# Performance work log

Hardware: AMD Instinct MI355X
Metric: run time of the kernel (lower is better)

## Reference

```python
import jax, jax.numpy as jnp
import numpy as np

N, R, D = 2048, 4, 256
TEMPERATURE = 1.0
CLAMP_MIN = 1e-8


def setup_inputs() -> dict:
    key = jax.random.key(0)
    a = jax.random.normal(key, (N, R, D), dtype=jnp.float32)
    return {"a": a}


def reference(a):
    n, r, d = a.shape
    # Full pairwise Gram tensor over (input i, context j) x (input k, context l)
    sim = jnp.einsum('ijd,kld->ikjl', a, a) / TEMPERATURE          # [N,N,r,r]
    # detached row-max over l for stability (matches sim.detach().max(-1, keepdim=True))
    sim_max = jax.lax.stop_gradient(jnp.max(sim, axis=-1, keepdims=True))
    dp = jnp.exp(sim - sim_max)                                    # [N,N,r,r]

    # Positive pairs: i == k, j != l
    diag = jnp.einsum('iijl->ijl', dp)                             # [N,r,r]
    offdiag_jl = ~jnp.eye(r, dtype=bool)                           # [r,r]
    sim_pos = jnp.sum(diag * offdiag_jl, axis=(1, 2)) / (r * (r - 1))  # [N]

    # Negative pairs: i != k, all (j,l); square then clamp, then per-i mean
    sq = jnp.maximum(jnp.square(dp), CLAMP_MIN)                    # [N,N,r,r]
    diag_sq = jnp.sum(jnp.maximum(jnp.square(diag), CLAMP_MIN), axis=(1, 2))  # [N]
    sim_neg = (jnp.sum(sq, axis=(1, 2, 3)) - diag_sq) / ((n - 1) * r * r)     # [N]

    lora_loss = -2.0 * sim_pos + sim_neg                           # [N]
    return jnp.mean(lora_loss)                                     # 'mean' reduction -> scalar
```

## Files before the change

### kernel.cpp

```cpp
#include <hip/hip_runtime.h>


#define PD   8192
#define KB   256
#define BM   128
#define BK   32
#define NIT  (KB / BK)

typedef __bf16 bf16x8 __attribute__((ext_vector_type(8)));
typedef float f32x4 __attribute__((ext_vector_type(4)));

__device__ __forceinline__ void gload16(const void* g, void* l) {
    __builtin_amdgcn_global_load_lds(
        (const __attribute__((address_space(1))) unsigned int*)g,
        (__attribute__((address_space(3))) unsigned int*)l, 16, 0, 0);
}

__device__ __forceinline__ int swz(int row) { return ((row >> 1) & 3) << 4; }

__device__ __forceinline__ float quadmax(float x) {
    int v = __builtin_amdgcn_mov_dpp(__builtin_bit_cast(int, x), 0xB1, 0xF, 0xF, true);
    float m = fmaxf(x, __builtin_bit_cast(float, v));
    v = __builtin_amdgcn_mov_dpp(__builtin_bit_cast(int, m), 0x4E, 0xF, 0xF, true);
    return fmaxf(m, __builtin_bit_cast(float, v));
}

__global__ __launch_bounds__(256)
void cvt_bf16(const float* __restrict__ A, __bf16* __restrict__ W,
              float* __restrict__ out) {
    const int idx = blockIdx.x * 256 + threadIdx.x;
    if (idx == 0) *out = 0.f;
    const float4 v0 = reinterpret_cast<const float4*>(A)[idx * 2];
    const float4 v1 = reinterpret_cast<const float4*>(A)[idx * 2 + 1];
    bf16x8 h;
    h[0] = (__bf16)v0.x; h[1] = (__bf16)v0.y; h[2] = (__bf16)v0.z; h[3] = (__bf16)v0.w;
    h[4] = (__bf16)v1.x; h[5] = (__bf16)v1.y; h[6] = (__bf16)v1.z; h[7] = (__bf16)v1.w;
    *reinterpret_cast<bf16x8*>(W + (size_t)idx * 8) = h;
}

__global__ __launch_bounds__(256)
void evd_mfma(const __bf16* __restrict__ W, float* __restrict__ out)
{
    __shared__ __bf16 lds[2][2][BM * BK];
    __shared__ float wsum[4];

    const int x = blockIdx.x, y = blockIdx.y;
    int bi, bk;
    if (x < 64 - y) { bi = y;      bk = y + x; }
    else            { bi = 63 - y; bk = x - 1; }

    const int tid = threadIdx.x;
    const int lane = tid & 63, wid = tid >> 6;
    const int wr = wid >> 1, wc = wid & 1;
    const int row0 = bi * BM, col0 = bk * BM;

    const int r0 = tid >> 2;
    const int r1 = 64 + r0;
    const int x0 = (tid & 3) * 16;
    const int ga0 = r0 * (KB * 2) + (x0 ^ swz(r0));
    const int ga1 = r1 * (KB * 2) + (x0 ^ swz(r1));
    const char* gAb = (const char*)(W + (size_t)row0 * KB);
    const char* gBb = (const char*)(W + (size_t)col0 * KB);
    const int ldsOff0 = wid * 1024;
    const int ldsOff1 = 4096 + wid * 1024;

    const int fr = lane & 15, kq = lane >> 4;
    int aOff[4], bOff[4];
#pragma unroll
    for (int m = 0; m < 4; ++m) {
        const int ra = wr * 64 + m * 16 + fr;
        const int rb = wc * 64 + m * 16 + fr;
        aOff[m] = ra * 64 + ((kq * 16) ^ swz(ra));
        bOff[m] = rb * 64 + ((kq * 16) ^ swz(rb));
    }

    f32x4 acc[4][4];
#pragma unroll
    for (int m = 0; m < 4; ++m)
#pragma unroll
        for (int n = 0; n < 4; ++n)
#pragma unroll
            for (int q = 0; q < 4; ++q) acc[m][n][q] = 0.f;

    auto stage = [&](int t, int b) {
        const int kbyte = t * (BK * 2);
        char* dA = (char*)&lds[b][0][0];
        char* dB = (char*)&lds[b][1][0];
        gload16(gAb + ga0 + kbyte, dA + ldsOff0);
        gload16(gAb + ga1 + kbyte, dA + ldsOff1);
        gload16(gBb + ga0 + kbyte, dB + ldsOff0);
        gload16(gBb + ga1 + kbyte, dB + ldsOff1);
    };

    stage(0, 0);
    stage(1, 1);

#pragma unroll
    for (int t = 0; t < NIT; ++t) {
        if (t == NIT - 1) asm volatile("s_waitcnt vmcnt(0)" ::: "memory");
        else              asm volatile("s_waitcnt vmcnt(4)" ::: "memory");
        __builtin_amdgcn_s_barrier();

        const char* baseA = (const char*)&lds[t & 1][0][0];
        const char* baseB = (const char*)&lds[t & 1][1][0];
        bf16x8 af[4], bfr[4];
#pragma unroll
        for (int m = 0; m < 4; ++m) {
            af[m]  = *(const bf16x8*)(baseA + aOff[m]);
            bfr[m] = *(const bf16x8*)(baseB + bOff[m]);
        }
        if (t + 2 < NIT) {
            asm volatile("s_waitcnt lgkmcnt(0)" ::: "memory");
            __builtin_amdgcn_s_barrier();
            stage(t + 2, t & 1);
        }
#pragma unroll
        for (int m = 0; m < 4; ++m)
#pragma unroll
            for (int n = 0; n < 4; ++n)
                acc[m][n] = __builtin_amdgcn_mfma_f32_16x16x32_bf16(af[m], bfr[n], acc[m][n], 0, 0, 0);
    }

    const float C_NEG = 1.0f / (2048.0f * 2047.0f * 16.0f);
    const float C_POS = 2.0f / (2048.0f * 12.0f);
    const float SCL = 2.0f * 1.4426950408889634f;
    const bool diag = (bi == bk);
    const bool ik = ((lane >> 4) == ((lane & 15) >> 2));
    float nsum = 0.f, psum = 0.f;

#pragma unroll
    for (int m = 0; m < 4; ++m) {
#pragma unroll
        for (int n = 0; n < 4; ++n) {
            float yv[4];
#pragma unroll
            for (int q = 0; q < 4; ++q) yv[q] = SCL * acc[m][n][q];
            const bool dfrag = diag && (wr == wc) && (m == n);
#pragma unroll
            for (int r = 0; r < 4; ++r) {
                const float d2 = yv[r] - quadmax(yv[r]);
                if (dfrag) {
                    const float dp = __builtin_amdgcn_exp2f(0.5f * d2);
                    if (ik) {
                        if (r != (lane & 3)) psum += dp;
                    } else {
                        nsum += fmaxf(dp * dp, 1e-8f);
                    }
                } else {
                    nsum += fmaxf(__builtin_amdgcn_exp2f(d2), 1e-8f);
                }
            }
            if (!diag) {
                const float ymax = fmaxf(fmaxf(fmaxf(yv[0], yv[1]), yv[2]), yv[3]);
#pragma unroll
                for (int r = 0; r < 4; ++r)
                    nsum += fmaxf(__builtin_amdgcn_exp2f(yv[r] - ymax), 1e-8f);
            }
        }
    }

    float contrib = C_NEG * nsum - C_POS * psum;

#pragma unroll
    for (int off = 32; off; off >>= 1) contrib += __shfl_down(contrib, off);
    if ((tid & 63) == 0) wsum[tid >> 6] = contrib;
    __syncthreads();
    if (tid == 0) atomicAdd(out, wsum[0] + wsum[1] + wsum[2] + wsum[3]);
}

extern "C" void kernel_launch(void* const* d_in, const int* in_sizes, int n_in,
                              void* d_out, int out_size, void* d_ws, size_t ws_size,
                              hipStream_t stream) {
    const float* A = (const float*)d_in[0];
    float* out = (float*)d_out;
    __bf16* W = (__bf16*)d_ws;
    cvt_bf16<<<(PD * KB / 8) / 256, 256, 0, stream>>>(A, W, out);
    dim3 grid(65, 32);
    evd_mfma<<<grid, 256, 0, stream>>>(W, out);
}
```

Baseline: 98.96 us.

## Use 8-wave blocks with 64x32 warp tiles, XCD-aware block remap, MFMA priority

Each 128x128 tile block now runs 8 waves instead of 4, and each wave computes a 64x32 sub-tile, which halves per-wave accumulators and increases latency hiding. The grid is flattened to 1D and remapped so consecutive blocks spread across the XCDs in chunks, aiming for better L2 locality. s_setprio is raised around the MFMA loop. Staging is simplified to one load per operand per thread. The cost is more waves contending for LDS and barriers, and a more complex epilogue diagonal test.

```diff
diff --git a/kernel.cpp b/kernel.cpp
--- a/kernel.cpp
+++ b/kernel.cpp
@@ -38,58 +38,49 @@
     *reinterpret_cast<bf16x8*>(W + (size_t)idx * 8) = h;
 }
 
-__global__ __launch_bounds__(256)
+__global__ __launch_bounds__(512, 4)
 void evd_mfma(const __bf16* __restrict__ W, float* __restrict__ out)
 {
     __shared__ __bf16 lds[2][2][BM * BK];
-    __shared__ float wsum[4];
+    __shared__ float wsum[8];
 
-    const int x = blockIdx.x, y = blockIdx.y;
+    const int nid = blockIdx.x;
+    const int id  = (nid & 7) * 260 + (nid >> 3);
+    const int x = id % 65, y = id / 65;
     int bi, bk;
     if (x < 64 - y) { bi = y;      bk = y + x; }
     else            { bi = 63 - y; bk = x - 1; }
 
     const int tid = threadIdx.x;
-    const int lane = tid & 63, wid = tid >> 6;
-    const int wr = wid >> 1, wc = wid & 1;
+    const int lane = tid & 63, w = tid >> 6;
+    const int wr = w >> 2, wc = w & 3;
     const int row0 = bi * BM, col0 = bk * BM;
 
-    const int r0 = tid >> 2;
-    const int r1 = 64 + r0;
-    const int x0 = (tid & 3) * 16;
-    const int ga0 = r0 * (KB * 2) + (x0 ^ swz(r0));
-    const int ga1 = r1 * (KB * 2) + (x0 ^ swz(r1));
-    const char* gAb = (const char*)(W + (size_t)row0 * KB);
-    const char* gBb = (const char*)(W + (size_t)col0 * KB);
-    const int ldsOff0 = wid * 1024;
-    const int ldsOff1 = 4096 + wid * 1024;
+    const int sr = w * 16 + (lane >> 2);
+    const int su = lane & 3;
+    const char* gW = (const char*)W;
+    const int gaA = (row0 + sr) * (KB * 2) + ((su * 16) ^ swz(sr));
+    const int gaB = (col0 + sr) * (KB * 2) + ((su * 16) ^ swz(sr));
+    const int dSt = w * 1024;
 
     const int fr = lane & 15, kq = lane >> 4;
-    int aOff[4], bOff[4];
-#pragma unroll
-    for (int m = 0; m < 4; ++m) {
-        const int ra = wr * 64 + m * 16 + fr;
-        const int rb = wc * 64 + m * 16 + fr;
-        aOff[m] = ra * 64 + ((kq * 16) ^ swz(ra));
-        bOff[m] = rb * 64 + ((kq * 16) ^ swz(rb));
-    }
+    const int sw = ((fr >> 1) & 3) << 4;
+    const int aBase = (wr * 64 + fr) * 64 + ((kq * 16) ^ sw);
+    const int bBase = 8192 + (wc * 32 + fr) * 64 + ((kq * 16) ^ sw);
 
-    f32x4 acc[4][4];
+    f32x4 acc[4][2];
 #pragma unroll
     for (int m = 0; m < 4; ++m)
 #pragma unroll
-        for (int n = 0; n < 4; ++n)
+        for (int n = 0; n < 2; ++n)
 #pragma unroll
             for (int q = 0; q < 4; ++q) acc[m][n][q] = 0.f;
 
-    auto stage = [&](int t, int b) {
-        const int kbyte = t * (BK * 2);
-        char* dA = (char*)&lds[b][0][0];
-        char* dB = (char*)&lds[b][1][0];
-        gload16(gAb + ga0 + kbyte, dA + ldsOff0);
-        gload16(gAb + ga1 + kbyte, dA + ldsOff1);
-        gload16(gBb + ga0 + kbyte, dB + ldsOff0);
-        gload16(gBb + ga1 + kbyte, dB + ldsOff1);
+    auto stage = [&](int c, int b) {
+        const int kb2 = c * (BK * 2);
+        char* base = (char*)&lds[b][0][0];
+        gload16(gW + gaA + kb2, base + dSt);
+        gload16(gW + gaB + kb2, base + 8192 + dSt);
     };
 
     stage(0, 0);
@@ -98,27 +89,29 @@
 #pragma unroll
     for (int t = 0; t < NIT; ++t) {
         if (t == NIT - 1) asm volatile("s_waitcnt vmcnt(0)" ::: "memory");
-        else              asm volatile("s_waitcnt vmcnt(4)" ::: "memory");
+        else              asm volatile("s_waitcnt vmcnt(2)" ::: "memory");
         __builtin_amdgcn_s_barrier();
 
-        const char* baseA = (const char*)&lds[t & 1][0][0];
-        const char* baseB = (const char*)&lds[t & 1][1][0];
-        bf16x8 af[4], bfr[4];
+        const char* base = (const char*)&lds[t & 1][0][0];
+        bf16x8 af[4], bf[2];
 #pragma unroll
-        for (int m = 0; m < 4; ++m) {
-            af[m]  = *(const bf16x8*)(baseA + aOff[m]);
-            bfr[m] = *(const bf16x8*)(baseB + bOff[m]);
-        }
+        for (int m = 0; m < 4; ++m)
+            af[m] = *(const bf16x8*)(base + aBase + m * 1024);
+#pragma unroll
+        for (int n = 0; n < 2; ++n)
+            bf[n] = *(const bf16x8*)(base + bBase + n * 1024);
         if (t + 2 < NIT) {
             asm volatile("s_waitcnt lgkmcnt(0)" ::: "memory");
             __builtin_amdgcn_s_barrier();
             stage(t + 2, t & 1);
         }
+        __builtin_amdgcn_s_setprio(1);
 #pragma unroll
         for (int m = 0; m < 4; ++m)
 #pragma unroll
-            for (int n = 0; n < 4; ++n)
-                acc[m][n] = __builtin_amdgcn_mfma_f32_16x16x32_bf16(af[m], bfr[n], acc[m][n], 0, 0, 0);
+            for (int n = 0; n < 2; ++n)
+                acc[m][n] = __builtin_amdgcn_mfma_f32_16x16x32_bf16(af[m], bf[n], acc[m][n], 0, 0, 0);
+        __builtin_amdgcn_s_setprio(0);
     }
 
     const float C_NEG = 1.0f / (2048.0f * 2047.0f * 16.0f);
@@ -131,11 +124,11 @@
 #pragma unroll
     for (int m = 0; m < 4; ++m) {
 #pragma unroll
-        for (int n = 0; n < 4; ++n) {
+        for (int n = 0; n < 2; ++n) {
             float yv[4];
 #pragma unroll
             for (int q = 0; q < 4; ++q) yv[q] = SCL * acc[m][n][q];
-            const bool dfrag = diag && (wr == wc) && (m == n);
+            const bool dfrag = diag && (wr * 4 + m == wc * 2 + n);
 #pragma unroll
             for (int r = 0; r < 4; ++r) {
                 const float d2 = yv[r] - quadmax(yv[r]);
@@ -163,9 +156,14 @@
 
 #pragma unroll
     for (int off = 32; off; off >>= 1) contrib += __shfl_down(contrib, off);
-    if ((tid & 63) == 0) wsum[tid >> 6] = contrib;
+    if (lane == 0) wsum[w] = contrib;
     __syncthreads();
-    if (tid == 0) atomicAdd(out, wsum[0] + wsum[1] + wsum[2] + wsum[3]);
+    if (tid == 0) {
+        float s = 0.f;
+#pragma unroll
+        for (int i = 0; i < 8; ++i) s += wsum[i];
+        atomicAdd(out, s);
+    }
 }
 
 extern "C" void kernel_launch(void* const* d_in, const int* in_sizes, int n_in,
@@ -175,6 +173,5 @@
     float* out = (float*)d_out;
     __bf16* W = (__bf16*)d_ws;
     cvt_bf16<<<(PD * KB / 8) / 256, 256, 0, stream>>>(A, W, out);
-    dim3 grid(65, 32);
-    evd_mfma<<<grid, 256, 0, stream>>>(W, out);
+    evd_mfma<<<2080, 512, 0, stream>>>(W, out);
 }
```

Result: no change. 97.58 us (-1.4%).
